# Optimization experiments

Measured on AMD Instinct MI355X. Metric: run time of the kernel, lower is better.

Reference implementation:

```python
import jax, jax.numpy as jnp
import numpy as np

H = 230  # temp_hidden
D = 2 * H  # encoded feature dim = 460


def _lstm(x, Wih, Whh, bih, bhh, reverse=False):
    # x: (B, T, Din) -> (B, T, H); PyTorch gate order i, f, g, o; zero init state
    B = x.shape[0]
    h0 = jnp.zeros((B, H), x.dtype)

    def step(carry, xt):
        h, c = carry
        g = xt @ Wih.T + h @ Whh.T + bih + bhh
        i, f, gg, o = jnp.split(g, 4, axis=-1)
        c = jax.nn.sigmoid(f) * c + jax.nn.sigmoid(i) * jnp.tanh(gg)
        h = jax.nn.sigmoid(o) * jnp.tanh(c)
        return (h, c), h

    _, hs = jax.lax.scan(step, (h0, h0), jnp.swapaxes(x, 0, 1), reverse=reverse)
    return jnp.swapaxes(hs, 0, 1)


def _bilstm(x, Wf, Uf, bf1, bf2, Wb, Ub, bb1, bb2):
    return jnp.concatenate([_lstm(x, Wf, Uf, bf1, bf2),
                            _lstm(x, Wb, Ub, bb1, bb2, reverse=True)], -1)


def _forward(p_features, q_features, score_w, score_b,
             m_Wih_f, m_Whh_f, m_bih_f, m_bhh_f,
             m_Wih_b, m_Whh_b, m_bih_b, m_bhh_b,
             w2a_w, w2a_b, w1a_w, w1a_b,
             b_Wih_f, b_Whh_f, b_bih_f, b_bhh_f,
             b_Wih_b, b_Whh_b, b_bih_b, b_bhh_b):
    # score(cat(p, q, p*q)) decomposed: u[p,q,b] = p.w_p + q.w_q + (p*q).w_pq + bias
    w_p, w_q, w_pq = score_w[0, :D], score_w[0, D:2 * D], score_w[0, 2 * D:]
    u = (jnp.einsum('pbd,d->pb', p_features, w_p)[:, None, :]
         + jnp.einsum('qbd,d->qb', q_features, w_q)[None, :, :]
         + jnp.einsum('pbd,qbd->pqb', p_features * w_pq, q_features)
         + score_b[0])  # (P, Q, B)

    q2c = jnp.transpose(jax.nn.softmax(u, axis=1), (2, 0, 1))  # (B, P, Q)
    c2q = jnp.max(u, axis=1).T                                   # (B, P)

    p_t = jnp.swapaxes(p_features, 0, 1)  # (B, P, D)
    q_t = jnp.swapaxes(q_features, 0, 1)  # (B, Q, D)
    new_u = jnp.einsum('bpq,bqd->bpd', q2c, q_t)  # (B, P, D)
    new_h = c2q[:, :, None] * p_t                  # (B, P, D)

    final_in = jnp.concatenate([p_t, new_h, p_t * new_u, p_t * new_h], -1)  # (B, P, 8H)
    final = _bilstm(final_in, m_Wih_f, m_Whh_f, m_bih_f, m_bhh_f,
                    m_Wih_b, m_Whh_b, m_bih_b, m_bhh_b)  # (B, P, 2H)

    def ptr_scores(h0a):  # h0a: (B, 2H) -> (B, P)
        cat = jnp.concatenate(
            [final, jnp.broadcast_to(h0a[:, None, :], final.shape)], -1)  # (B, P, 4H)
        z = jnp.tanh(jnp.einsum('bpd,ed->bpe', cat, w2a_w) + w2a_b)
        return jnp.einsum('bpe,e->bp', z, w1a_w[0]) + w1a_b[0]

    Bsz = final.shape[0]
    s1 = ptr_scores(jnp.zeros((Bsz, 2 * H), final.dtype))
    alpha1 = jax.nn.softmax(s1, axis=1)                       # (B, P)
    c1 = jnp.einsum('bp,bpd->bd', alpha1, final)[:, None, :]  # (B, 1, 2H)
    h0a = _bilstm(c1, b_Wih_f, b_Whh_f, b_bih_f, b_bhh_f,
                  b_Wih_b, b_Whh_b, b_bih_b, b_bhh_b)[:, 0, :]  # (B, 2H)
    alpha2 = jax.nn.log_softmax(ptr_scores(h0a), axis=1)
    return final, jnp.log(alpha1), alpha2


def setup_inputs() -> dict:
    key = jax.random.key(0)
    ks = jax.random.split(key, 24)
    P, Q, B = 512, 64, 32
    s = 0.05

    def rn(k, shape):
        return jax.random.normal(k, shape, jnp.float32) * s

    return {
        'p_features': jax.random.normal(ks[0], (P, B, D), jnp.float32),
        'q_features': jax.random.normal(ks[1], (Q, B, D), jnp.float32),
        'score_w': rn(ks[2], (1, 3 * D)), 'score_b': rn(ks[3], (1,)),
        'm_Wih_f': rn(ks[4], (4 * H, 8 * H)), 'm_Whh_f': rn(ks[5], (4 * H, H)),
        'm_bih_f': rn(ks[6], (4 * H,)), 'm_bhh_f': rn(ks[7], (4 * H,)),
        'm_Wih_b': rn(ks[8], (4 * H, 8 * H)), 'm_Whh_b': rn(ks[9], (4 * H, H)),
        'm_bih_b': rn(ks[10], (4 * H,)), 'm_bhh_b': rn(ks[11], (4 * H,)),
        'w2a_w': rn(ks[12], (2 * H, 4 * H)), 'w2a_b': rn(ks[13], (2 * H,)),
        'w1a_w': rn(ks[14], (1, 2 * H)), 'w1a_b': rn(ks[15], (1,)),
        'b_Wih_f': rn(ks[16], (4 * H, 2 * H)), 'b_Whh_f': rn(ks[17], (4 * H, H)),
        'b_bih_f': rn(ks[18], (4 * H,)), 'b_bhh_f': rn(ks[19], (4 * H,)),
        'b_Wih_b': rn(ks[20], (4 * H, 2 * H)), 'b_Whh_b': rn(ks[21], (4 * H, H)),
        'b_bih_b': rn(ks[22], (4 * H,)), 'b_bhh_b': rn(ks[23], (4 * H,)),
    }


def reference(p_features, q_features, score_w, score_b,
              m_Wih_f, m_Whh_f, m_bih_f, m_bhh_f,
              m_Wih_b, m_Whh_b, m_bih_b, m_bhh_b,
              w2a_w, w2a_b, w1a_w, w1a_b,
              b_Wih_f, b_Whh_f, b_bih_f, b_bhh_f,
              b_Wih_b, b_Whh_b, b_bih_b, b_bhh_b):
    return _forward(p_features, q_features, score_w, score_b,
                    m_Wih_f, m_Whh_f, m_bih_f, m_bhh_f,
                    m_Wih_b, m_Whh_b, m_bih_b, m_bhh_b,
                    w2a_w, w2a_b, w1a_w, w1a_b,
                    b_Wih_f, b_Whh_f, b_bih_f, b_bhh_f,
                    b_Wih_b, b_Whh_b, b_bih_b, b_bhh_b)
```

## Files before the change

kernel.cpp:

```cpp
#include <hip/hip_runtime.h>

#define HH 230
#define DD 460
#define PPn 512
#define QQn 64
#define BBn 32
#define G4 920
#define K1 1840
#define KP1 1856
#define MRn 16384
#define KP3 480
#define LDFB 480

typedef _Float16 f16;
typedef f16 half2v __attribute__((ext_vector_type(2)));
typedef short bf16x8_t __attribute__((ext_vector_type(8)));
typedef float f32x4_t __attribute__((ext_vector_type(4)));

__device__ __forceinline__ float sigm(float x) { return 1.0f / (1.0f + __expf(-x)); }
__device__ __forceinline__ float tanhfast(float x) { return 1.0f - 2.0f / (__expf(2.0f * x) + 1.0f); }

__device__ __forceinline__ unsigned short f2bf(float x) {
  unsigned int u = __builtin_bit_cast(unsigned int, x);
  unsigned int r = (u + 0x7fffu + ((u >> 16) & 1u)) >> 16;
  return (unsigned short)r;
}
__device__ __forceinline__ float bf2f(unsigned short h) {
  unsigned int u = ((unsigned int)h) << 16;
  return __builtin_bit_cast(float, u);
}

__device__ __forceinline__ float dot2f(half2v a, half2v b, float c) {
#if __has_builtin(__builtin_amdgcn_fdot2)
  return __builtin_amdgcn_fdot2(a, b, c, false);
#else
  return c + (float)a.x * (float)b.x + (float)a.y * (float)b.y;
#endif
}
__device__ __forceinline__ half2v bch2(unsigned int u) { return __builtin_bit_cast(half2v, u); }

static constexpr size_t SZ_X   = (size_t)MRn * G4 * 4;
static constexpr size_t OFF_XF = 0;
static constexpr size_t OFF_XB = OFF_XF + SZ_X;
static constexpr size_t OFF_FI = OFF_XB + SZ_X;
static constexpr size_t SZ_FI  = (size_t)MRn * KP1 * 2;
static constexpr size_t OFF_Y  = OFF_FI;
static constexpr size_t OFF_FB = OFF_FI + (size_t)MRn * DD * 4;
static constexpr size_t OFF_WFP = OFF_FI + SZ_FI;
static constexpr size_t SZ_WP1  = (size_t)1024 * KP1 * 2;
static constexpr size_t OFF_WBP = OFF_WFP + SZ_WP1;
static constexpr size_t OFF_W2P = OFF_WBP + SZ_WP1;
static constexpr size_t SZ_W2P  = (size_t)512 * KP3 * 2;
static constexpr size_t OFF_WPF = OFF_W2P + SZ_W2P;
static constexpr size_t SZ_WPK  = (size_t)115 * G4 * 4;
static constexpr size_t OFF_WPB = ((OFF_WPF + SZ_WPK + 255) & ~(size_t)255);
static constexpr size_t OFF_WTF = ((OFF_WPB + SZ_WPK + 255) & ~(size_t)255);
static constexpr size_t SZ_WT   = (size_t)DD * G4 * 4;
static constexpr size_t OFF_WTB = OFF_WTF + SZ_WT;
static constexpr size_t OFF_BIASF = OFF_WTB + SZ_WT;
static constexpr size_t OFF_BIASB = ((OFF_BIASF + G4 * 4 + 255) & ~(size_t)255);
static constexpr size_t OFF_SP  = ((OFF_BIASB + G4 * 4 + 255) & ~(size_t)255);
static constexpr size_t OFF_SQ  = OFF_SP + (size_t)PPn * BBn * 4;
static constexpr size_t OFF_S1  = OFF_SQ + (size_t)QQn * BBn * 4;
static constexpr size_t OFF_AL1 = OFF_S1 + (size_t)MRn * 4;
static constexpr size_t OFF_C1  = OFF_AL1 + (size_t)MRn * 4;
static constexpr size_t OFF_H0A = ((OFF_C1 + (size_t)BBn * DD * 4 + 255) & ~(size_t)255);
static constexpr size_t OFF_HR  = ((OFF_H0A + (size_t)BBn * DD * 4 + 255) & ~(size_t)255);
static constexpr size_t OFF_S2  = ((OFF_HR + (size_t)BBn * DD * 4 + 255) & ~(size_t)255);

__global__ __launch_bounds__(256) void k_pad_wih(const float* __restrict__ Wf, const float* __restrict__ Wb,
                                                 unsigned short* __restrict__ Pf, unsigned short* __restrict__ Pb) {
  size_t idx = (size_t)blockIdx.x * 256 + threadIdx.x;
  int n = (int)(idx / KP1), k = (int)(idx % KP1);
  const float* W = blockIdx.y ? Wb : Wf;
  unsigned short* Pp = blockIdx.y ? Pb : Pf;
  float v = (n < G4 && k < K1) ? W[(size_t)n * K1 + k] : 0.f;
  Pp[idx] = f2bf(v);
}

__global__ __launch_bounds__(256) void k_pad_w2a(const float* __restrict__ W, unsigned short* __restrict__ Pq) {
  size_t idx = (size_t)blockIdx.x * 256 + threadIdx.x;
  int n = (int)(idx / KP3), k = (int)(idx % KP3);
  float v = (n < DD && k < DD) ? W[(size_t)n * G4 + k] : 0.f;
  Pq[idx] = f2bf(v);
}

__global__ __launch_bounds__(256) void k_pack_whh(const float* __restrict__ Wf, const float* __restrict__ Wb,
                                                  unsigned int* __restrict__ Pf, unsigned int* __restrict__ Pb) {
  int idx = blockIdx.x * 256 + threadIdx.x;
  if (idx >= 115 * G4) return;
  int kk = idx / G4, row = idx % G4;
  const float* W = blockIdx.y ? Wb : Wf;
  unsigned int* Pp = blockIdx.y ? Pb : Pf;
  half2v h; h.x = (f16)W[(size_t)row * HH + 2 * kk]; h.y = (f16)W[(size_t)row * HH + 2 * kk + 1];
  Pp[idx] = __builtin_bit_cast(unsigned int, h);
}

__global__ __launch_bounds__(256) void k_pack_bwih(const float* __restrict__ Wf, const float* __restrict__ Wb,
                                                   float* __restrict__ Tf, float* __restrict__ Tb) {
  int idx = blockIdx.x * 256 + threadIdx.x;
  if (idx >= DD * G4) return;
  int d = idx / G4, row = idx % G4;
  const float* W = blockIdx.y ? Wb : Wf;
  float* T = blockIdx.y ? Tb : Tf;
  T[idx] = W[(size_t)row * DD + d];
}

__global__ __launch_bounds__(256) void k_bias(const float* __restrict__ bihF, const float* __restrict__ bhhF,
                                              const float* __restrict__ bihB, const float* __restrict__ bhhB,
                                              float* __restrict__ biasF, float* __restrict__ biasB) {
  int i = blockIdx.x * 256 + threadIdx.x;
  if (i < G4) {
    if (blockIdx.y == 0) biasF[i] = bihF[i] + bhhF[i];
    else biasB[i] = bihB[i] + bhhB[i];
  }
}

__global__ __launch_bounds__(256) void k_fbpad(unsigned short* __restrict__ FB) {
  int i = blockIdx.x * 256 + threadIdx.x;
  int r = i / 20, j = i % 20;
  FB[(size_t)r * LDFB + DD + j] = 0;
}

__global__ __launch_bounds__(256) void k_rowdot(const float* __restrict__ M, const float* __restrict__ w,
                                                float* __restrict__ out) {
  int r = blockIdx.x * 4 + (threadIdx.x >> 6);
  int lane = threadIdx.x & 63;
  const float* row = M + (size_t)r * DD;
  float acc = 0.f;
  for (int d = lane; d < DD; d += 64) acc += row[d] * w[d];
#pragma unroll
  for (int d = 1; d < 64; d <<= 1) acc += __shfl_xor(acc, d, 64);
  if (lane == 0) out[r] = acc;
}

__global__ __launch_bounds__(256) void k_attn(const float* __restrict__ p_feat, const float* __restrict__ q_feat,
                                              const float* __restrict__ score_w, const float* __restrict__ score_b,
                                              const float* __restrict__ sp, const float* __restrict__ sq,
                                              unsigned short* __restrict__ FIp) {
  __shared__ half2v q_s[64 * 230];
  __shared__ half2v p_s[32 * 230];
  __shared__ half2v wpq[230];
  __shared__ float sq_s[64];
  __shared__ float u_row[64];
  __shared__ __align__(16) float w_row[64];
  __shared__ float mxs[1];

  int tid = threadIdx.x;
  int b = blockIdx.y;
  int p0 = blockIdx.x * 32;

  for (int i = tid; i < 230; i += 256) {
    half2v w; w.x = (f16)score_w[2 * DD + 2 * i]; w.y = (f16)score_w[2 * DD + 2 * i + 1];
    wpq[i] = w;
  }
  for (int i = tid; i < 64; i += 256) sq_s[i] = sq[i * BBn + b];
  for (int q = 0; q < 64; q++) {
    for (int i = tid; i < 230; i += 256) {
      float2 f2 = *(const float2*)(q_feat + ((size_t)(q * BBn + b)) * DD + 2 * i);
      half2v v; v.x = (f16)f2.x; v.y = (f16)f2.y;
      q_s[q * 230 + i] = v;
    }
  }
  for (int pl = 0; pl < 32; pl++) {
    for (int i = tid; i < 230; i += 256) {
      float2 f2 = *(const float2*)(p_feat + ((size_t)((p0 + pl) * BBn + b)) * DD + 2 * i);
      half2v v; v.x = (f16)f2.x; v.y = (f16)f2.y;
      p_s[pl * 230 + i] = v;
    }
  }
  __syncthreads();

  float sbias = score_b[0];
  int lane = tid & 63, wv = tid >> 6;
  int myq = tid >> 2, quarter = tid & 3;
  int kb = quarter * 58;
  int ke = (kb + 58 < 230) ? (kb + 58) : 230;

  for (int pl = 0; pl < 32; pl++) {
    float acc = 0.f;
    const half2v* prow = p_s + pl * 230;
    const half2v* qrow = q_s + myq * 230;
    for (int k = kb; k < ke; k++) {
      half2v pw = prow[k] * wpq[k];
      acc = dot2f(pw, qrow[k], acc);
    }
    acc += __shfl_xor(acc, 1, 64);
    acc += __shfl_xor(acc, 2, 64);
    if (quarter == 0) u_row[myq] = acc + sp[(p0 + pl) * BBn + b] + sq_s[myq] + sbias;
    __syncthreads();
    if (wv == 0) {
      float v = u_row[lane];
      float m = v;
#pragma unroll
      for (int d = 1; d < 64; d <<= 1) m = fmaxf(m, __shfl_xor(m, d, 64));
      float e = __expf(v - m);
      float s = e;
#pragma unroll
      for (int d = 1; d < 64; d <<= 1) s += __shfl_xor(s, d, 64);
      w_row[lane] = e / s;
      if (lane == 0) mxs[0] = m;
    }
    __syncthreads();
    if (tid < 230) {
      float c2q = mxs[0];
      half2v pv = p_s[pl * 230 + tid];
      float nux = 0.f, nuy = 0.f;
      for (int q = 0; q < 64; q += 4) {
        float4 wq = *(const float4*)&w_row[q];
        half2v q0 = q_s[(q + 0) * 230 + tid];
        half2v q1 = q_s[(q + 1) * 230 + tid];
        half2v q2 = q_s[(q + 2) * 230 + tid];
        half2v q3 = q_s[(q + 3) * 230 + tid];
        nux = fmaf(wq.x, (float)q0.x, nux); nuy = fmaf(wq.x, (float)q0.y, nuy);
        nux = fmaf(wq.y, (float)q1.x, nux); nuy = fmaf(wq.y, (float)q1.y, nuy);
        nux = fmaf(wq.z, (float)q2.x, nux); nuy = fmaf(wq.z, (float)q2.y, nuy);
        nux = fmaf(wq.w, (float)q3.x, nux); nuy = fmaf(wq.w, (float)q3.y, nuy);
      }
      float px = (float)pv.x, py = (float)pv.y;
      size_t rr = (size_t)(b * PPn + p0 + pl);
      unsigned short* o = FIp + rr * KP1 + 2 * tid;
      *(unsigned int*)(o +    0) = (unsigned int)f2bf(px)            | ((unsigned int)f2bf(py) << 16);
      *(unsigned int*)(o +  460) = (unsigned int)f2bf(c2q * px)      | ((unsigned int)f2bf(c2q * py) << 16);
      *(unsigned int*)(o +  920) = (unsigned int)f2bf(px * nux)      | ((unsigned int)f2bf(py * nuy) << 16);
      *(unsigned int*)(o + 1380) = (unsigned int)f2bf(c2q * px * px) | ((unsigned int)f2bf(c2q * py * py) << 16);
    } else if (tid < 238) {
      int j = tid - 230;
      size_t rr = (size_t)(b * PPn + p0 + pl);
      *(unsigned int*)(FIp + rr * KP1 + 1840 + 2 * j) = 0u;
    }
    __syncthreads();
  }
}

__global__ __launch_bounds__(256, 2) void k_gemm(const unsigned short* __restrict__ A, int lda,
                                                 const unsigned short* __restrict__ Bw, int ldb,
                                                 float* __restrict__ C, int ldc,
                                                 int Nreal, int Ktiles, const float* __restrict__ bias) {
  __shared__ unsigned short As[128 * 32];
  __shared__ unsigned short Bs[128 * 32];
  int tid = threadIdx.x;
  int m0 = blockIdx.x * 128, n0 = blockIdx.y * 128;
  int wv = tid >> 6, lane = tid & 63;
  int wr = wv >> 1, wc = wv & 1;
  int laneM = lane & 15, laneK = lane >> 4;

  f32x4_t acc[4][4];
#pragma unroll
  for (int i = 0; i < 4; i++)
#pragma unroll
    for (int j = 0; j < 4; j++) acc[i][j] = (f32x4_t){0.f, 0.f, 0.f, 0.f};

  int row0 = tid >> 2, ch0 = tid & 3;
  int row1 = (256 + tid) >> 2, ch1 = tid & 3;
  const unsigned short* a0 = A + (size_t)(m0 + row0) * lda + ch0 * 8;
  const unsigned short* a1 = A + (size_t)(m0 + row1) * lda + ch1 * 8;
  const unsigned short* b0 = Bw + (size_t)(n0 + row0) * ldb + ch0 * 8;
  const unsigned short* b1 = Bw + (size_t)(n0 + row1) * ldb + ch1 * 8;

  for (int kt = 0; kt < Ktiles; kt++) {
    uint4 av0 = *(const uint4*)a0;
    uint4 av1 = *(const uint4*)a1;
    uint4 bv0 = *(const uint4*)b0;
    uint4 bv1 = *(const uint4*)b1;
    a0 += 32; a1 += 32; b0 += 32; b1 += 32;
    __syncthreads();
    *(uint4*)(As + (size_t)tid * 8)         = av0;
    *(uint4*)(As + (size_t)(256 + tid) * 8) = av1;
    *(uint4*)(Bs + (size_t)tid * 8)         = bv0;
    *(uint4*)(Bs + (size_t)(256 + tid) * 8) = bv1;
    __syncthreads();
    bf16x8_t af[4], bfr[4];
#pragma unroll
    for (int mi = 0; mi < 4; mi++)
      af[mi] = *(const bf16x8_t*)(As + (size_t)(wr * 64 + mi * 16 + laneM) * 32 + laneK * 8);
#pragma unroll
    for (int ni = 0; ni < 4; ni++)
      bfr[ni] = *(const bf16x8_t*)(Bs + (size_t)(wc * 64 + ni * 16 + laneM) * 32 + laneK * 8);
#pragma unroll
    for (int mi = 0; mi < 4; mi++)
#pragma unroll
      for (int ni = 0; ni < 4; ni++)
        acc[mi][ni] = __builtin_amdgcn_mfma_f32_16x16x32_bf16(af[mi], bfr[ni], acc[mi][ni], 0, 0, 0);
  }
#pragma unroll
  for (int mi = 0; mi < 4; mi++)
#pragma unroll
    for (int ni = 0; ni < 4; ni++) {
      int ccol = n0 + wc * 64 + ni * 16 + laneM;
      if (ccol < Nreal) {
        float bv = bias ? bias[ccol] : 0.f;
#pragma unroll
        for (int j = 0; j < 4; j++) {
          int crow = m0 + wr * 64 + mi * 16 + laneK * 4 + j;
          C[(size_t)crow * ldc + ccol] = acc[mi][ni][j] + bv;
        }
      }
    }
}

__global__ __launch_bounds__(960, 1)
void k_recur(const unsigned int* __restrict__ WPf,
             const unsigned int* __restrict__ WPb,
             const float* __restrict__ Xf, const float* __restrict__ Xb,
             float* __restrict__ outF, unsigned short* __restrict__ FB) {
  __shared__ unsigned int wlds[920 * 12];
  __shared__ unsigned int h2[2][116];
  __shared__ float gbuf[3][232];
  int tid = threadIdx.x;
  int dir = blockIdx.x >> 5, b = blockIdx.x & 31;
  const unsigned int* __restrict__ WP = dir ? WPb : WPf;
  const float* __restrict__ X = dir ? Xb : Xf;

  bool act = tid < 920;
  int row = tid;
  int gate = row / 230;
  int u = row - gate * 230;

  half2v w[104];
  if (act) {
#pragma unroll
    for (int k = 0; k < 104; k++) w[k] = bch2(WP[k * G4 + row]);
    unsigned int* sl = &wlds[row * 12];
#pragma unroll
    for (int j = 0; j < 11; j++) sl[j] = WP[(104 + j) * G4 + row];
    sl[11] = 0u;
  }
  for (int i = tid; i < 116; i += 960) { h2[0][i] = 0u; h2[1][i] = 0u; }

  float x0 = 0.f;
  if (act) x0 = X[(size_t)(b * PPn + (dir ? PPn - 1 : 0)) * G4 + row];
  float c = 0.f;
  __syncthreads();

  for (int s = 0; s < PPn; s++) {
    int t = dir ? (PPn - 1 - s) : s;
    float acc = x0;
    if (act && s < PPn - 1) {
      int tn = dir ? (PPn - 2 - s) : (s + 1);
      x0 = X[(size_t)(b * PPn + tn) * G4 + row];
    }
    const unsigned int* hb = h2[s & 1];
    if (act) {
#pragma unroll
      for (int ch = 0; ch < 26; ch++) {
        uint4 hv = *(const uint4*)(hb + ch * 4);
        acc = dot2f(w[ch * 4 + 0], bch2(hv.x), acc);
        acc = dot2f(w[ch * 4 + 1], bch2(hv.y), acc);
        acc = dot2f(w[ch * 4 + 2], bch2(hv.z), acc);
        acc = dot2f(w[ch * 4 + 3], bch2(hv.w), acc);
      }
      const unsigned int* sl = &wlds[row * 12];
#pragma unroll
      for (int j = 0; j < 3; j++) {
        uint4 wv = *(const uint4*)(sl + 4 * j);
        uint4 hv = *(const uint4*)(hb + 104 + 4 * j);
        acc = dot2f(bch2(wv.x), bch2(hv.x), acc);
        acc = dot2f(bch2(wv.y), bch2(hv.y), acc);
        acc = dot2f(bch2(wv.z), bch2(hv.z), acc);
        acc = dot2f(bch2(wv.w), bch2(hv.w), acc);
      }
      if (gate == 0)      gbuf[0][u] = sigm(acc);
      else if (gate == 1) gbuf[1][u] = sigm(acc);
      else if (gate == 2) gbuf[2][u] = tanhfast(acc);
    }
    __syncthreads();
    if (act && gate == 3) {
      c = gbuf[1][u] * c + gbuf[0][u] * gbuf[2][u];
      float hval = sigm(acc) * tanhfast(c);
      f16* hw = (f16*)(&h2[(s + 1) & 1][0]);
      hw[u] = (f16)hval;
      size_t ro = (size_t)(b * PPn + t);
      outF[ro * DD + dir * HH + u] = hval;
      FB[ro * LDFB + dir * HH + u] = f2bf(hval);
    }
    __syncthreads();
  }
}

__global__ __launch_bounds__(256) void k_score(const float* __restrict__ Yv, const float* __restrict__ hR,
                                               const float* __restrict__ w1a, const float* __restrict__ w1b,
                                               float* __restrict__ out) {
  int r = blockIdx.x * 4 + (threadIdx.x >> 6);
  int lane = threadIdx.x & 63;
  const float* row = Yv + (size_t)r * DD;
  const float* hrow = hR ? (hR + (size_t)(r >> 9) * DD) : nullptr;
  float acc = 0.f;
  for (int e = lane; e < DD; e += 64) {
    float v = row[e];
    if (hrow) v += hrow[e];
    acc += tanhfast(v) * w1a[e];
  }
#pragma unroll
  for (int d = 1; d < 64; d <<= 1) acc += __shfl_xor(acc, d, 64);
  if (lane == 0) out[r] = acc + w1b[0];
}

__global__ __launch_bounds__(512) void k_softmax(const float* __restrict__ s, float* __restrict__ outLog,
                                                 float* __restrict__ outAlpha) {
  __shared__ float red[8];
  int b = blockIdx.x, t = threadIdx.x;
  int lane = t & 63, wv = t >> 6;
  float v = s[b * PPn + t];
  float m = v;
#pragma unroll
  for (int d = 1; d < 64; d <<= 1) m = fmaxf(m, __shfl_xor(m, d, 64));
  if (lane == 0) red[wv] = m;
  __syncthreads();
  float mall = red[0];
#pragma unroll
  for (int i = 1; i < 8; i++) mall = fmaxf(mall, red[i]);
  __syncthreads();
  float e = __expf(v - mall);
  float sum = e;
#pragma unroll
  for (int d = 1; d < 64; d <<= 1) sum += __shfl_xor(sum, d, 64);
  if (lane == 0) red[wv] = sum;
  __syncthreads();
  float tot = red[0];
#pragma unroll
  for (int i = 1; i < 8; i++) tot += red[i];
  float lz = __logf(tot);
  outLog[b * PPn + t] = v - mall - lz;
  if (outAlpha) outAlpha[b * PPn + t] = e / tot;
}

__global__ __launch_bounds__(256) void k_c1(const float* __restrict__ alpha1, const float* __restrict__ finalF,
                                            float* __restrict__ c1) {
  __shared__ float al[512];
  int b = blockIdx.x, t = threadIdx.x;
  al[t] = alpha1[b * PPn + t];
  al[t + 256] = alpha1[b * PPn + t + 256];
  __syncthreads();
  for (int d = t; d < DD; d += 256) {
    float acc = 0.f;
#pragma unroll 8
    for (int p = 0; p < PPn; p++) acc += al[p] * finalF[((size_t)b * PPn + p) * DD + d];
    c1[b * DD + d] = acc;
  }
}

__global__ __launch_bounds__(256) void k_h0a(const float* __restrict__ WTf, const float* __restrict__ WTb,
                                             const float* __restrict__ bihF, const float* __restrict__ bhhF,
                                             const float* __restrict__ bihB, const float* __restrict__ bhhB,
                                             const float* __restrict__ c1, float* __restrict__ h0a) {
  int dir = blockIdx.x >> 5, b = blockIdx.x & 31;
  const float* WT = dir ? WTb : WTf;
  const float* bih = dir ? bihB : bihF;
  const float* bhh = dir ? bhhB : bhhF;
  __shared__ float cs[DD];
  int t = threadIdx.x;
  for (int d = t; d < DD; d += 256) cs[d] = c1[b * DD + d];
  __syncthreads();
  if (t < HH) {
    float gi = bih[t] + bhh[t];
    float gg = bih[2 * HH + t] + bhh[2 * HH + t];
    float go = bih[3 * HH + t] + bhh[3 * HH + t];
    for (int d = 0; d < DD; d++) {
      float cv = cs[d];
      const float* wr2 = WT + (size_t)d * G4;
      gi = fmaf(cv, wr2[t], gi);
      gg = fmaf(cv, wr2[2 * HH + t], gg);
      go = fmaf(cv, wr2[3 * HH + t], go);
    }
    float cc = sigm(gi) * tanhfast(gg);
    h0a[b * DD + dir * HH + t] = sigm(go) * tanhfast(cc);
  }
}

__global__ __launch_bounds__(256) void k_hR(const float* __restrict__ w2a_w, const float* __restrict__ h0a,
                                            float* __restrict__ hR) {
  int b = blockIdx.x, t = threadIdx.x;
  __shared__ float hs[DD];
  for (int d = t; d < DD; d += 256) hs[d] = h0a[b * DD + d];
  __syncthreads();
  for (int e = t; e < DD; e += 256) {
    float acc = 0.f;
    const float* wr2 = w2a_w + (size_t)e * G4 + DD;
    for (int d = 0; d < DD; d++) acc = fmaf(hs[d], wr2[d], acc);
    hR[b * DD + e] = acc;
  }
}

extern "C" void kernel_launch(void* const* d_in, const int* in_sizes, int n_in,
                              void* d_out, int out_size, void* d_ws, size_t ws_size,
                              hipStream_t stream) {
  (void)in_sizes; (void)n_in; (void)out_size; (void)ws_size;
  const float* p_feat  = (const float*)d_in[0];
  const float* q_feat  = (const float*)d_in[1];
  const float* score_w = (const float*)d_in[2];
  const float* score_b = (const float*)d_in[3];
  const float* mWihF   = (const float*)d_in[4];
  const float* mWhhF   = (const float*)d_in[5];
  const float* mBihF   = (const float*)d_in[6];
  const float* mBhhF   = (const float*)d_in[7];
  const float* mWihB   = (const float*)d_in[8];
  const float* mWhhB   = (const float*)d_in[9];
  const float* mBihB   = (const float*)d_in[10];
  const float* mBhhB   = (const float*)d_in[11];
  const float* w2a_w   = (const float*)d_in[12];
  const float* w2a_b   = (const float*)d_in[13];
  const float* w1a_w   = (const float*)d_in[14];
  const float* w1a_b   = (const float*)d_in[15];
  const float* bWihF   = (const float*)d_in[16];
  const float* bBihF   = (const float*)d_in[18];
  const float* bBhhF   = (const float*)d_in[19];
  const float* bWihB   = (const float*)d_in[20];
  const float* bBihB   = (const float*)d_in[22];
  const float* bBhhB   = (const float*)d_in[23];

  char* ws = (char*)d_ws;
  float* XF = (float*)(ws + OFF_XF);
  float* XB = (float*)(ws + OFF_XB);
  unsigned short* FI = (unsigned short*)(ws + OFF_FI);
  float* Yv = (float*)(ws + OFF_Y);
  unsigned short* FB = (unsigned short*)(ws + OFF_FB);
  unsigned short* WFP = (unsigned short*)(ws + OFF_WFP);
  unsigned short* WBP = (unsigned short*)(ws + OFF_WBP);
  unsigned short* W2P = (unsigned short*)(ws + OFF_W2P);
  unsigned int* WPF = (unsigned int*)(ws + OFF_WPF);
  unsigned int* WPB = (unsigned int*)(ws + OFF_WPB);
  float* WTF = (float*)(ws + OFF_WTF);
  float* WTB = (float*)(ws + OFF_WTB);
  float* BIASF = (float*)(ws + OFF_BIASF);
  float* BIASB = (float*)(ws + OFF_BIASB);
  float* SP = (float*)(ws + OFF_SP);
  float* SQ = (float*)(ws + OFF_SQ);
  float* S1 = (float*)(ws + OFF_S1);
  float* AL1 = (float*)(ws + OFF_AL1);
  float* C1 = (float*)(ws + OFF_C1);
  float* H0A = (float*)(ws + OFF_H0A);
  float* HR = (float*)(ws + OFF_HR);
  float* S2 = (float*)(ws + OFF_S2);

  float* outF = (float*)d_out;
  float* outLA1 = outF + (size_t)BBn * PPn * DD;
  float* outA2 = outLA1 + (size_t)BBn * PPn;

  k_pad_wih<<<dim3(7424, 2), 256, 0, stream>>>(mWihF, mWihB, WFP, WBP);
  k_pad_w2a<<<dim3(960), 256, 0, stream>>>(w2a_w, W2P);
  k_pack_whh<<<dim3(414, 2), 256, 0, stream>>>(mWhhF, mWhhB, WPF, WPB);
  k_pack_bwih<<<dim3(1654, 2), 256, 0, stream>>>(bWihF, bWihB, WTF, WTB);
  k_bias<<<dim3(4, 2), 256, 0, stream>>>(mBihF, mBhhF, mBihB, mBhhB, BIASF, BIASB);
  k_fbpad<<<dim3(1280), 256, 0, stream>>>(FB);
  k_rowdot<<<dim3(4096), 256, 0, stream>>>(p_feat, score_w, SP);
  k_rowdot<<<dim3(512), 256, 0, stream>>>(q_feat, score_w + DD, SQ);
  k_attn<<<dim3(16, 32), 256, 0, stream>>>(p_feat, q_feat, score_w, score_b, SP, SQ, FI);
  k_gemm<<<dim3(128, 8), 256, 0, stream>>>(FI, KP1, WFP, KP1, XF, G4, G4, 58, BIASF);
  k_gemm<<<dim3(128, 8), 256, 0, stream>>>(FI, KP1, WBP, KP1, XB, G4, G4, 58, BIASB);
  k_recur<<<dim3(64), 960, 0, stream>>>(WPF, WPB, XF, XB, outF, FB);
  k_gemm<<<dim3(128, 4), 256, 0, stream>>>(FB, KP3, W2P, KP3, Yv, DD, DD, 15, w2a_b);
  k_score<<<dim3(4096), 256, 0, stream>>>(Yv, nullptr, w1a_w, w1a_b, S1);
  k_softmax<<<dim3(32), 512, 0, stream>>>(S1, outLA1, AL1);
  k_c1<<<dim3(32), 256, 0, stream>>>(AL1, outF, C1);
  k_h0a<<<dim3(64), 256, 0, stream>>>(WTF, WTB, bBihF, bBhhF, bBihB, bBhhB, C1, H0A);
  k_hR<<<dim3(32), 256, 0, stream>>>(w2a_w, H0A, HR);
  k_score<<<dim3(4096), 256, 0, stream>>>(Yv, HR, w1a_w, w1a_b, S2);
  k_softmax<<<dim3(32), 512, 0, stream>>>(S2, outA2, nullptr);
}
```

Baseline: 1.602 ms.

## Split each LSTM recurrence chain across two workgroups with flag-based h exchange

The recurrent LSTM kernel now runs each (direction, batch) chain on two workgroups of 512 threads, each owning half of the hidden units, instead of one 960-thread workgroup. At every timestep each half publishes its new hidden values to global memory, raises a step flag, spins until the partner's flag arrives, then pulls the partner's half into LDS. The goal is to halve per-thread dot-product work and use twice as many CUs on the latency-bound serial recurrence. In exchange every step pays a cross-CU global-memory handshake and extra barriers, and the kernel relies on both partner workgroups being resident at the same time.

After: 6.116 ms. 282% more time.

```diff
diff --git a/kernel.cpp b/kernel.cpp
--- a/kernel.cpp
+++ b/kernel.cpp
@@ -24,10 +24,6 @@
   unsigned int u = __builtin_bit_cast(unsigned int, x);
   unsigned int r = (u + 0x7fffu + ((u >> 16) & 1u)) >> 16;
   return (unsigned short)r;
-}
-__device__ __forceinline__ float bf2f(unsigned short h) {
-  unsigned int u = ((unsigned int)h) << 16;
-  return __builtin_bit_cast(float, u);
 }
 
 __device__ __forceinline__ float dot2f(half2v a, half2v b, float c) {
@@ -67,6 +63,8 @@
 static constexpr size_t OFF_H0A = ((OFF_C1 + (size_t)BBn * DD * 4 + 255) & ~(size_t)255);
 static constexpr size_t OFF_HR  = ((OFF_H0A + (size_t)BBn * DD * 4 + 255) & ~(size_t)255);
 static constexpr size_t OFF_S2  = ((OFF_HR + (size_t)BBn * DD * 4 + 255) & ~(size_t)255);
+static constexpr size_t OFF_FLG = ((OFF_S2 + (size_t)MRn * 4 + 255) & ~(size_t)255);
+static constexpr size_t OFF_HX  = OFF_FLG + 128 * 64;
 
 __global__ __launch_bounds__(256) void k_pad_wih(const float* __restrict__ Wf, const float* __restrict__ Wb,
                                                  unsigned short* __restrict__ Pf, unsigned short* __restrict__ Pb) {
@@ -120,6 +118,10 @@
   int i = blockIdx.x * 256 + threadIdx.x;
   int r = i / 20, j = i % 20;
   FB[(size_t)r * LDFB + DD + j] = 0;
+}
+
+__global__ __launch_bounds__(256) void k_zflags(unsigned int* __restrict__ flg) {
+  flg[blockIdx.x * 256 + threadIdx.x] = 0;
 }
 
 __global__ __launch_bounds__(256) void k_rowdot(const float* __restrict__ M, const float* __restrict__ w,
@@ -299,80 +301,110 @@
     }
 }
 
-__global__ __launch_bounds__(960, 1)
+__global__ __launch_bounds__(512, 1)
 void k_recur(const unsigned int* __restrict__ WPf,
              const unsigned int* __restrict__ WPb,
              const float* __restrict__ Xf, const float* __restrict__ Xb,
-             float* __restrict__ outF, unsigned short* __restrict__ FB) {
-  __shared__ unsigned int wlds[920 * 12];
+             float* __restrict__ outF, unsigned short* __restrict__ FB,
+             unsigned int* __restrict__ hx, unsigned int* __restrict__ flg) {
+  __shared__ unsigned int wlds[460 * 28];
   __shared__ unsigned int h2[2][116];
-  __shared__ float gbuf[3][232];
+  __shared__ float gbuf[3][116];
   int tid = threadIdx.x;
-  int dir = blockIdx.x >> 5, b = blockIdx.x & 31;
+  int wgid = blockIdx.x;
+  int chain = wgid >> 1;
+  int half = wgid & 1;
+  int dir = chain >> 5, b = chain & 31;
   const unsigned int* __restrict__ WP = dir ? WPb : WPf;
   const float* __restrict__ X = dir ? Xb : Xf;
 
-  bool act = tid < 920;
-  int row = tid;
-  int gate = row / 230;
-  int u = row - gate * 230;
-
-  half2v w[104];
+  bool act = tid < 460;
+  int gate = tid / 115;
+  int uL = tid - gate * 115;
+  int u = half * 115 + uL;
+  int row = gate * 230 + u;
+
+  half2v w[88];
   if (act) {
 #pragma unroll
-    for (int k = 0; k < 104; k++) w[k] = bch2(WP[k * G4 + row]);
-    unsigned int* sl = &wlds[row * 12];
-#pragma unroll
-    for (int j = 0; j < 11; j++) sl[j] = WP[(104 + j) * G4 + row];
-    sl[11] = 0u;
-  }
-  for (int i = tid; i < 116; i += 960) { h2[0][i] = 0u; h2[1][i] = 0u; }
+    for (int k = 0; k < 88; k++) w[k] = bch2(WP[k * G4 + row]);
+    unsigned int* sl = &wlds[tid * 28];
+#pragma unroll
+    for (int j = 0; j < 27; j++) sl[j] = WP[(88 + j) * G4 + row];
+    sl[27] = 0u;
+  }
+  for (int i = tid; i < 116; i += 512) { h2[0][i] = 0u; h2[1][i] = 0u; }
 
   float x0 = 0.f;
   if (act) x0 = X[(size_t)(b * PPn + (dir ? PPn - 1 : 0)) * G4 + row];
   float c = 0.f;
+
+  unsigned int* hx_mine    = hx + (size_t)wgid * 256;
+  const unsigned int* hx_p = hx + (size_t)(wgid ^ 1) * 256;
+  unsigned int* flg_mine   = flg + wgid * 16;
+  unsigned int* flg_p      = flg + (wgid ^ 1) * 16;
   __syncthreads();
 
   for (int s = 0; s < PPn; s++) {
     int t = dir ? (PPn - 1 - s) : s;
+    int par = s & 1;
     float acc = x0;
     if (act && s < PPn - 1) {
       int tn = dir ? (PPn - 2 - s) : (s + 1);
       x0 = X[(size_t)(b * PPn + tn) * G4 + row];
     }
-    const unsigned int* hb = h2[s & 1];
+    const unsigned int* hb = h2[par];
     if (act) {
 #pragma unroll
-      for (int ch = 0; ch < 26; ch++) {
+      for (int ch = 0; ch < 22; ch++) {
         uint4 hv = *(const uint4*)(hb + ch * 4);
         acc = dot2f(w[ch * 4 + 0], bch2(hv.x), acc);
         acc = dot2f(w[ch * 4 + 1], bch2(hv.y), acc);
         acc = dot2f(w[ch * 4 + 2], bch2(hv.z), acc);
         acc = dot2f(w[ch * 4 + 3], bch2(hv.w), acc);
       }
-      const unsigned int* sl = &wlds[row * 12];
-#pragma unroll
-      for (int j = 0; j < 3; j++) {
+      const unsigned int* sl = &wlds[tid * 28];
+#pragma unroll
+      for (int j = 0; j < 7; j++) {
         uint4 wv = *(const uint4*)(sl + 4 * j);
-        uint4 hv = *(const uint4*)(hb + 104 + 4 * j);
+        uint4 hv = *(const uint4*)(hb + 88 + 4 * j);
         acc = dot2f(bch2(wv.x), bch2(hv.x), acc);
         acc = dot2f(bch2(wv.y), bch2(hv.y), acc);
         acc = dot2f(bch2(wv.z), bch2(hv.z), acc);
         acc = dot2f(bch2(wv.w), bch2(hv.w), acc);
       }
-      if (gate == 0)      gbuf[0][u] = sigm(acc);
-      else if (gate == 1) gbuf[1][u] = sigm(acc);
-      else if (gate == 2) gbuf[2][u] = tanhfast(acc);
+      if (gate == 0)      gbuf[0][uL] = sigm(acc);
+      else if (gate == 1) gbuf[1][uL] = sigm(acc);
+      else if (gate == 2) gbuf[2][uL] = tanhfast(acc);
     }
     __syncthreads();
     if (act && gate == 3) {
-      c = gbuf[1][u] * c + gbuf[0][u] * gbuf[2][u];
+      c = gbuf[1][uL] * c + gbuf[0][uL] * gbuf[2][uL];
       float hval = sigm(acc) * tanhfast(c);
-      f16* hw = (f16*)(&h2[(s + 1) & 1][0]);
-      hw[u] = (f16)hval;
+      f16 hf = (f16)hval;
+      unsigned short hbits = __builtin_bit_cast(unsigned short, hf);
+      ((unsigned short*)&h2[par ^ 1][0])[u] = hbits;
+      __hip_atomic_store(&hx_mine[par * 128 + uL], (unsigned int)hbits,
+                         __ATOMIC_RELAXED, __HIP_MEMORY_SCOPE_AGENT);
+      __threadfence();
       size_t ro = (size_t)(b * PPn + t);
       outF[ro * DD + dir * HH + u] = hval;
       FB[ro * LDFB + dir * HH + u] = f2bf(hval);
+    }
+    __syncthreads();
+    if (tid == 0) {
+      __hip_atomic_store(flg_mine, (unsigned int)(s + 1),
+                         __ATOMIC_RELEASE, __HIP_MEMORY_SCOPE_AGENT);
+      while (__hip_atomic_load(flg_p, __ATOMIC_ACQUIRE, __HIP_MEMORY_SCOPE_AGENT)
+             < (unsigned int)(s + 1)) {
+        __builtin_amdgcn_s_sleep(2);
+      }
+    }
+    __syncthreads();
+    if (tid < 115) {
+      unsigned int hv = __hip_atomic_load(&hx_p[par * 128 + tid],
+                                          __ATOMIC_RELAXED, __HIP_MEMORY_SCOPE_AGENT);
+      ((unsigned short*)&h2[par ^ 1][0])[(1 - half) * 115 + tid] = (unsigned short)hv;
     }
     __syncthreads();
   }
@@ -532,6 +564,8 @@
   float* H0A = (float*)(ws + OFF_H0A);
   float* HR = (float*)(ws + OFF_HR);
   float* S2 = (float*)(ws + OFF_S2);
+  unsigned int* FLG = (unsigned int*)(ws + OFF_FLG);
+  unsigned int* HX  = (unsigned int*)(ws + OFF_HX);
 
   float* outF = (float*)d_out;
   float* outLA1 = outF + (size_t)BBn * PPn * DD;
@@ -543,12 +577,13 @@
   k_pack_bwih<<<dim3(1654, 2), 256, 0, stream>>>(bWihF, bWihB, WTF, WTB);
   k_bias<<<dim3(4, 2), 256, 0, stream>>>(mBihF, mBhhF, mBihB, mBhhB, BIASF, BIASB);
   k_fbpad<<<dim3(1280), 256, 0, stream>>>(FB);
+  k_zflags<<<dim3(8), 256, 0, stream>>>(FLG);
   k_rowdot<<<dim3(4096), 256, 0, stream>>>(p_feat, score_w, SP);
   k_rowdot<<<dim3(512), 256, 0, stream>>>(q_feat, score_w + DD, SQ);
   k_attn<<<dim3(16, 32), 256, 0, stream>>>(p_feat, q_feat, score_w, score_b, SP, SQ, FI);
   k_gemm<<<dim3(128, 8), 256, 0, stream>>>(FI, KP1, WFP, KP1, XF, G4, G4, 58, BIASF);
   k_gemm<<<dim3(128, 8), 256, 0, stream>>>(FI, KP1, WBP, KP1, XB, G4, G4, 58, BIASB);
-  k_recur<<<dim3(64), 960, 0, stream>>>(WPF, WPB, XF, XB, outF, FB);
+  k_recur<<<dim3(128), 512, 0, stream>>>(WPF, WPB, XF, XB, outF, FB, HX, FLG);
   k_gemm<<<dim3(128, 4), 256, 0, stream>>>(FB, KP3, W2P, KP3, Yv, DD, DD, 15, w2a_b);
   k_score<<<dim3(4096), 256, 0, stream>>>(Yv, nullptr, w1a_w, w1a_b, S1);
   k_softmax<<<dim3(32), 512, 0, stream>>>(S1, outLA1, AL1);
```
